# Optimization experiments

Hardware: AMD Instinct MI355X
Metric: run time of the kernel (lower is better)

Reference implementation:

```python
import jax, jax.numpy as jnp
import numpy as np

B, S, D = 4, 2048, 1024
HALF_PI = np.float32(np.pi / 2.0)


def setup_inputs() -> dict:
    key = jax.random.key(0)
    ks = jax.random.split(key, 12)
    std = np.float32(0.02)
    def w(k):
        return jax.random.normal(k, (D, D), dtype=jnp.float32) * std
    return {
        "x": jax.random.normal(ks[0], (B, S, D), dtype=jnp.float32),
        "W_q": w(ks[1]), "b_q": jnp.zeros((D,), jnp.float32),
        "W_k": w(ks[2]), "b_k": jnp.zeros((D,), jnp.float32),
        "W_v": w(ks[3]), "b_v": jnp.zeros((D,), jnp.float32),
        "W_t": w(ks[4]), "b_t": jnp.zeros((D,), jnp.float32),
        "W_o": w(ks[5]), "b_o": jnp.zeros((D,), jnp.float32),
        "entangle_strength": jnp.float32(0.5),
    }


def reference(x, W_q, b_q, W_k, b_k, W_v, b_v, W_t, b_t, W_o, b_o, entangle_strength):
    scale = jnp.float32(np.sqrt(D))
    Q = x @ W_q + b_q          # [B,S,D]
    K = x @ W_k + b_k
    V = x @ W_v + b_v
    # theta in [0, pi/2]; r = cos(2*theta)
    theta_q = jax.nn.sigmoid(Q @ W_t + b_t) * HALF_PI
    theta_k = jax.nn.sigmoid(K @ W_t + b_t) * HALF_PI
    r_q = jnp.cos(2.0 * theta_q)
    r_k = jnp.cos(2.0 * theta_k)
    classical = jnp.einsum("bqd,bkd->bqk", Q, K) / scale
    quantum = jnp.einsum("bqd,bkd->bqk", r_q, r_k) * entangle_strength
    attn_weights = jax.nn.softmax(classical + quantum, axis=-1)  # [B,S,S]
    # dropout: eval mode -> identity
    out = jnp.einsum("bqk,bkd->bqd", attn_weights, V)
    out = out @ W_o + b_o
    return out, attn_weights
```

## Files before the change

kernel.cpp:

```cpp
#include <hip/hip_runtime.h>
#include <cstdint>

typedef unsigned short u16;
typedef __attribute__((ext_vector_type(8))) short bf16x8;
typedef __attribute__((ext_vector_type(4))) float f32x4;

__device__ __forceinline__ u16 f2b(float x) {
  unsigned u = __float_as_uint(x);
  u += 0x7FFFu + ((u >> 16) & 1u);
  return (u16)(u >> 16);
}

__device__ __forceinline__ void gload16(const void* g, void* l) {
  __builtin_amdgcn_global_load_lds(
      (const __attribute__((address_space(1))) void*)g,
      (__attribute__((address_space(3))) void*)l, 16, 0, 0);
}

__device__ __forceinline__ int swz(int r) { return (r & 3) ^ ((r >> 2) & 3); }

template <int N>
__device__ __forceinline__ void vmwait() {
  if constexpr (N == 0) asm volatile("s_waitcnt vmcnt(0)" ::: "memory");
  else if constexpr (N == 3) asm volatile("s_waitcnt vmcnt(3)" ::: "memory");
  else if constexpr (N == 4) asm volatile("s_waitcnt vmcnt(4)" ::: "memory");
  else if constexpr (N == 6) asm volatile("s_waitcnt vmcnt(6)" ::: "memory");
  else if constexpr (N == 8) asm volatile("s_waitcnt vmcnt(8)" ::: "memory");
}

template <int L>
__device__ __forceinline__ void stage_region(const u16* __restrict__ G,
                                             long long ld, int gcol,
                                             u16* L_, int tid) {
#pragma unroll
  for (int j = 0; j < L; ++j) {
    const int P = j * 512 + tid;
    const int r = P >> 2;
    const int cl = (P & 3) ^ swz(r);
    gload16(G + (long long)r * ld + gcol + cl * 8, L_ + P * 8);
  }
}

__device__ __forceinline__ bf16x8 frag(const u16* reg_, int row, int cA) {
  return *(const bf16x8*)(reg_ + row * 32 + ((cA ^ swz(row)) << 3));
}

template <int EPI, int WM, int WN, int MR, int NR>
__global__ __launch_bounds__(512, 2) void g8p(
    const u16* __restrict__ A, long long lda, long long sAz,
    const u16* __restrict__ B, long long ldb, long long sBz,
    void* __restrict__ C0, void* __restrict__ C1, void* __restrict__ C2,
    long long ldc, long long sCz, int K,
    const float* __restrict__ b0, const float* __restrict__ b1,
    const float* __restrict__ b2, float preScale, const float* __restrict__ esp) {
  constexpr int BM = WM * MR * 16, BN = WN * NR * 16;
  constexpr int LA = BM / 128, LB = BN / 128;
  constexpr int AHALF = BM * 32;
  constexpr int BHALF = BN * 32;
  constexpr int BUFU = 2 * (AHALF + BHALF);
  constexpr int NH = NR / 2;
  __shared__ __align__(16) u16 lds[2 * BUFU];

  const int gx = gridDim.x, S = gx * gridDim.y;
  const int hw = blockIdx.y * gx + blockIdx.x;
  const int l = (hw & 7) * (S >> 3) + (hw >> 3);
  const int bx = l % gx, by = l / gx;
  const int z = blockIdx.z;
  const long long tM = (long long)by * BM;
  const long long tN = (long long)bx * BN;
  const u16* Ab = A + z * sAz + tM * lda;
  const u16* Bb = B + z * sBz + tN * ldb;
  const int tid = threadIdx.x;
  const int NT = K >> 6;

  stage_region<LA>(Ab, lda, 0,  lds, tid);
  stage_region<LB>(Bb, ldb, 0,  lds + 2 * AHALF, tid);
  stage_region<LA>(Ab, lda, 32, lds + AHALF, tid);
  stage_region<LB>(Bb, ldb, 32, lds + 2 * AHALF + BHALF, tid);
  stage_region<LA>(Ab, lda, 64, lds + BUFU, tid);
  stage_region<LB>(Bb, ldb, 64, lds + BUFU + 2 * AHALF, tid);
  vmwait<2 * (LA + LB)>();
  __builtin_amdgcn_s_barrier();

  const int wid = tid >> 6, lane = tid & 63;
  const int wm = wid / WN, wn = wid % WN;
  const int wr = wm * MR * 16, wc = wn * NR * 16;
  const int lr = lane & 15, cA = lane >> 4;
  f32x4 acc[MR][NR] = {};

  for (int t = 0; t < NT; ++t) {
    u16* bufc = lds + (t & 1) * BUFU;
    u16* bufn = lds + ((t + 1) & 1) * BUFU;
    const u16* Ak0p = bufc;
    const u16* Ak1p = bufc + AHALF;
    const u16* Bk0p = bufc + 2 * AHALF;
    const u16* Bk1p = bufc + 2 * AHALF + BHALF;
    bf16x8 a[MR], b[NH];

#pragma unroll
    for (int m = 0; m < MR; ++m) a[m] = frag(Ak0p, wr + m * 16 + lr, cA);
#pragma unroll
    for (int n = 0; n < NH; ++n) b[n] = frag(Bk0p, wc + n * 16 + lr, cA);
    if (t + 1 < NT)
      stage_region<LA>(Ab, lda, (t + 1) * 64 + 32, bufn + AHALF, tid);
    __builtin_amdgcn_s_barrier();
    asm volatile("s_waitcnt lgkmcnt(0)" ::: "memory");
    __builtin_amdgcn_s_setprio(1);
#pragma unroll
    for (int m = 0; m < MR; ++m)
#pragma unroll
      for (int n = 0; n < NH; ++n)
        acc[m][n] = __builtin_amdgcn_mfma_f32_16x16x32_bf16(a[m], b[n],
                                                            acc[m][n], 0, 0, 0);
    __builtin_amdgcn_s_setprio(0);
    __builtin_amdgcn_s_barrier();

#pragma unroll
    for (int n = 0; n < NH; ++n) b[n] = frag(Bk0p, wc + (NH + n) * 16 + lr, cA);
    if (t + 1 < NT)
      stage_region<LB>(Bb, ldb, (t + 1) * 64 + 32, bufn + 2 * AHALF + BHALF, tid);
    if (t < NT - 1) vmwait<2 * (LA + LB)>(); else vmwait<0>();
    __builtin_amdgcn_s_barrier();
    asm volatile("s_waitcnt lgkmcnt(0)" ::: "memory");
    __builtin_amdgcn_s_setprio(1);
#pragma unroll
    for (int m = 0; m < MR; ++m)
#pragma unroll
      for (int n = 0; n < NH; ++n)
        acc[m][NH + n] = __builtin_amdgcn_mfma_f32_16x16x32_bf16(
            a[m], b[n], acc[m][NH + n], 0, 0, 0);
    __builtin_amdgcn_s_setprio(0);
    __builtin_amdgcn_s_barrier();

#pragma unroll
    for (int m = 0; m < MR; ++m) a[m] = frag(Ak1p, wr + m * 16 + lr, cA);
#pragma unroll
    for (int n = 0; n < NH; ++n) b[n] = frag(Bk1p, wc + n * 16 + lr, cA);
    if (t + 2 < NT)
      stage_region<LA>(Ab, lda, (t + 2) * 64, bufc, tid);
    __builtin_amdgcn_s_barrier();
    asm volatile("s_waitcnt lgkmcnt(0)" ::: "memory");
    __builtin_amdgcn_s_setprio(1);
#pragma unroll
    for (int m = 0; m < MR; ++m)
#pragma unroll
      for (int n = 0; n < NH; ++n)
        acc[m][n] = __builtin_amdgcn_mfma_f32_16x16x32_bf16(a[m], b[n],
                                                            acc[m][n], 0, 0, 0);
    __builtin_amdgcn_s_setprio(0);
    __builtin_amdgcn_s_barrier();

#pragma unroll
    for (int n = 0; n < NH; ++n) b[n] = frag(Bk1p, wc + (NH + n) * 16 + lr, cA);
    if (t + 2 < NT)
      stage_region<LB>(Bb, ldb, (t + 2) * 64, bufc + 2 * AHALF, tid);
    if (t < NT - 2) vmwait<2 * (LA + LB)>();
    else if (t == NT - 2) vmwait<LA + LB>();
    __builtin_amdgcn_s_barrier();
    asm volatile("s_waitcnt lgkmcnt(0)" ::: "memory");
    __builtin_amdgcn_s_setprio(1);
#pragma unroll
    for (int m = 0; m < MR; ++m)
#pragma unroll
      for (int n = 0; n < NH; ++n)
        acc[m][NH + n] = __builtin_amdgcn_mfma_f32_16x16x32_bf16(
            a[m], b[n], acc[m][NH + n], 0, 0, 0);
    __builtin_amdgcn_s_setprio(0);
    __builtin_amdgcn_s_barrier();
  }

  const int rr = (lane >> 4) << 2;
  float ps = preScale, mul = 1.0f;
  if constexpr (EPI == 1) {
    ps = (z == 0) ? preScale : 1.0f;
    mul = (z == 0) ? esp[0] : 1.0f;
  }
#pragma unroll
  for (int m = 0; m < MR; ++m) {
#pragma unroll
    for (int n = 0; n < NR; ++n) {
      const int col = (int)tN + wc + n * 16 + lr;
#pragma unroll
      for (int r = 0; r < 4; ++r) {
        const long long row = tM + wr + m * 16 + rr + r;
        const float v = acc[m][n][r];
        if constexpr (EPI == 0) {
          const int g = col >> 10, cc = col & 1023;
          if (g == 0)      ((u16*)C0)[row * 2048 + cc] = f2b((v + b0[cc]) * 0.03125f);
          else if (g == 1) ((u16*)C1)[row * 2048 + cc] = f2b(v + b1[cc]);
          else             ((u16*)C2)[row * 1024 + cc] = f2b(v + b2[cc]);
        } else if constexpr (EPI == 1) {
          const float tt = v * ps + b0[col];
          const float sg = 1.f / (1.f + __expf(-tt));
          ((u16*)C0)[z * sCz + row * ldc + col] = f2b(mul * cospif(sg));
        } else if constexpr (EPI == 2) {
          ((u16*)C0)[z * sCz + row * ldc + col] = f2b(v);
        } else if constexpr (EPI == 3) {
          ((float*)C0)[z * sCz + row * ldc + col] = v + b0[col];
        } else {
          ((float*)C0)[z * sCz + row * ldc + col] = v;
        }
      }
    }
  }
}

__global__ __launch_bounds__(256) void softmax_rows(float* __restrict__ L,
                                                    u16* __restrict__ AB) {
  const long long row = blockIdx.x;
  float4* p4 = (float4*)(L + row * 2048);
  const int tid = threadIdx.x;
  float4 a = p4[tid], b = p4[tid + 256];
  float m = fmaxf(fmaxf(fmaxf(a.x, a.y), fmaxf(a.z, a.w)),
                  fmaxf(fmaxf(b.x, b.y), fmaxf(b.z, b.w)));
#pragma unroll
  for (int o = 32; o > 0; o >>= 1) m = fmaxf(m, __shfl_xor(m, o));
  __shared__ float rmax[4], rsum[4];
  const int wid = tid >> 6, lane = tid & 63;
  if (lane == 0) rmax[wid] = m;
  __syncthreads();
  m = fmaxf(fmaxf(rmax[0], rmax[1]), fmaxf(rmax[2], rmax[3]));
  a.x = __expf(a.x - m); a.y = __expf(a.y - m);
  a.z = __expf(a.z - m); a.w = __expf(a.w - m);
  b.x = __expf(b.x - m); b.y = __expf(b.y - m);
  b.z = __expf(b.z - m); b.w = __expf(b.w - m);
  float s = a.x + a.y + a.z + a.w + b.x + b.y + b.z + b.w;
#pragma unroll
  for (int o = 32; o > 0; o >>= 1) s += __shfl_xor(s, o);
  if (lane == 0) rsum[wid] = s;
  __syncthreads();
  s = rsum[0] + rsum[1] + rsum[2] + rsum[3];
  const float inv = 1.0f / s;
  a.x *= inv; a.y *= inv; a.z *= inv; a.w *= inv;
  b.x *= inv; b.y *= inv; b.z *= inv; b.w *= inv;
  p4[tid] = a;
  p4[tid + 256] = b;
  ushort4* o4 = (ushort4*)(AB + row * 2048);
  o4[tid]       = make_ushort4(f2b(a.x), f2b(a.y), f2b(a.z), f2b(a.w));
  o4[tid + 256] = make_ushort4(f2b(b.x), f2b(b.y), f2b(b.z), f2b(b.w));
}

__global__ __launch_bounds__(256) void cvt_x(const float* __restrict__ X,
                                             u16* __restrict__ XB) {
  const int i = blockIdx.x * 256 + threadIdx.x;
  float4 v = ((const float4*)X)[i];
  ((ushort4*)XB)[i] = make_ushort4(f2b(v.x), f2b(v.y), f2b(v.z), f2b(v.w));
}

__global__ void cvt_w(const float* __restrict__ W0, const float* __restrict__ W1,
                      const float* __restrict__ W2, const float* __restrict__ W3,
                      const float* __restrict__ W4, u16* __restrict__ WT) {
  __shared__ float t[32][33];
  const int z = blockIdx.z;
  const float* W = (z == 0) ? W0 : (z == 1) ? W1 : (z == 2) ? W2 : (z == 3) ? W3 : W4;
  u16* D = WT + (long long)z * 1024 * 1024;
  const int c0 = blockIdx.x * 32, r0 = blockIdx.y * 32;
  const int tx = threadIdx.x, ty = threadIdx.y;
#pragma unroll
  for (int i = 0; i < 4; ++i)
    t[ty + i * 8][tx] = W[(long long)(r0 + ty + i * 8) * 1024 + c0 + tx];
  __syncthreads();
#pragma unroll
  for (int i = 0; i < 4; ++i)
    D[(long long)(c0 + ty + i * 8) * 1024 + r0 + tx] = f2b(t[tx][ty + i * 8]);
}

__global__ void transpose_v(const u16* __restrict__ Vb, u16* __restrict__ VT) {
  __shared__ u16 t[32][33];
  const int b = blockIdx.z;
  const u16* V = Vb + (long long)b * 2048 * 1024;
  u16* O = VT + (long long)b * 1024 * 2048;
  const int d0 = blockIdx.x * 32, s0 = blockIdx.y * 32;
  const int tx = threadIdx.x, ty = threadIdx.y;
#pragma unroll
  for (int i = 0; i < 4; ++i)
    t[ty + i * 8][tx] = V[(long long)(s0 + ty + i * 8) * 1024 + d0 + tx];
  __syncthreads();
#pragma unroll
  for (int i = 0; i < 4; ++i)
    O[(long long)(d0 + ty + i * 8) * 2048 + s0 + tx] = t[tx][ty + i * 8];
}

extern "C" void kernel_launch(void* const* d_in, const int* in_sizes, int n_in,
                              void* d_out, int out_size, void* d_ws,
                              size_t ws_size, hipStream_t stream) {
  const float* x  = (const float*)d_in[0];
  const float* Wq = (const float*)d_in[1];
  const float* bq = (const float*)d_in[2];
  const float* Wk = (const float*)d_in[3];
  const float* bk = (const float*)d_in[4];
  const float* Wv = (const float*)d_in[5];
  const float* bv = (const float*)d_in[6];
  const float* Wt = (const float*)d_in[7];
  const float* bt = (const float*)d_in[8];
  const float* Wo = (const float*)d_in[9];
  const float* bo = (const float*)d_in[10];
  const float* es = (const float*)d_in[11];

  char* ws = (char*)d_ws;
  u16* WT   = (u16*)(ws);
  u16* XB   = (u16*)(ws + 10485760);
  u16* Qcat = (u16*)(ws + 27262976);
  u16* Kcat = Qcat + 16777216;
  u16* Vb   = (u16*)(ws + 94371840);
  u16* VT   = (u16*)(ws + 111149056);
  u16* WtT  = WT + 3 * 1048576;
  u16* WoT  = WT + 4 * 1048576;
  u16* ATT  = Qcat;
  u16* AV   = XB;

  float* outO = (float*)d_out;
  float* outA = outO + 8388608;

  cvt_x<<<8192, 256, 0, stream>>>(x, XB);
  cvt_w<<<dim3(32, 32, 5), dim3(32, 8), 0, stream>>>(Wq, Wk, Wv, Wt, Wo, WT);
  g8p<0, 4, 2, 2, 8><<<dim3(12, 64, 1), 512, 0, stream>>>(
      XB, 1024, 0, WT, 1024, 0, Qcat, Kcat, Vb, 0, 0, 1024, bq, bk, bv, 1.f, nullptr);
  g8p<1, 4, 2, 2, 8><<<dim3(4, 64, 2), 512, 0, stream>>>(
      Qcat, 2048, 16777216LL, WtT, 1024, 0, Qcat + 1024, nullptr, nullptr,
      2048, 16777216LL, 1024, bt, nullptr, nullptr, 32.f, es);
  transpose_v<<<dim3(32, 64, 4), dim3(32, 8), 0, stream>>>(Vb, VT);
  g8p<4, 2, 4, 8, 4><<<dim3(8, 8, 4), 512, 0, stream>>>(
      Qcat, 2048, 4194304LL, Kcat, 2048, 4194304LL, outA, nullptr, nullptr,
      2048, 4194304LL, 2048, nullptr, nullptr, nullptr, 1.f, nullptr);
  softmax_rows<<<8192, 256, 0, stream>>>(outA, ATT);
  g8p<2, 4, 2, 2, 8><<<dim3(4, 16, 4), 512, 0, stream>>>(
      ATT, 2048, 4194304LL, VT, 2048, 2097152LL, AV, nullptr, nullptr,
      1024, 2097152LL, 2048, nullptr, nullptr, nullptr, 1.f, nullptr);
  g8p<3, 4, 2, 2, 8><<<dim3(4, 64, 1), 512, 0, stream>>>(
      AV, 1024, 0, WoT, 1024, 0, outO, nullptr, nullptr,
      1024, 0, 1024, bo, nullptr, nullptr, 1.f, nullptr);
}
```

Baseline: 372.1 us.

## Restructure GEMM into quadrant-split tiles with 64-wide K chunks and 8-way swizzle

New measurement: 343.1 us. 7.8% less time.

```diff
diff --git a/kernel.cpp b/kernel.cpp
--- a/kernel.cpp
+++ b/kernel.cpp
@@ -16,8 +16,6 @@
       (const __attribute__((address_space(1))) void*)g,
       (__attribute__((address_space(3))) void*)l, 16, 0, 0);
 }
-
-__device__ __forceinline__ int swz(int r) { return (r & 3) ^ ((r >> 2) & 3); }
 
 template <int N>
 __device__ __forceinline__ void vmwait() {
@@ -29,37 +27,148 @@
 }
 
 template <int L>
-__device__ __forceinline__ void stage_region(const u16* __restrict__ G,
-                                             long long ld, int gcol,
-                                             u16* L_, int tid) {
+__device__ __forceinline__ void stage_half(const u16* __restrict__ G,
+                                           long long ld, int kb,
+                                           u16* Ldst, int tid) {
 #pragma unroll
   for (int j = 0; j < L; ++j) {
     const int P = j * 512 + tid;
-    const int r = P >> 2;
-    const int cl = (P & 3) ^ swz(r);
-    gload16(G + (long long)r * ld + gcol + cl * 8, L_ + P * 8);
-  }
-}
-
-__device__ __forceinline__ bf16x8 frag(const u16* reg_, int row, int cA) {
-  return *(const bf16x8*)(reg_ + row * 32 + ((cA ^ swz(row)) << 3));
-}
-
-template <int EPI, int WM, int WN, int MR, int NR>
-__global__ __launch_bounds__(512, 2) void g8p(
+    const int r = P >> 3, c = P & 7;
+    gload16(G + (long long)r * ld + kb + ((c ^ (r & 7)) << 3), Ldst + P * 8);
+  }
+}
+
+__device__ __forceinline__ bf16x8 fr8(const u16* R, int row, int chunk) {
+  return *(const bf16x8*)(R + row * 64 + ((chunk ^ (row & 7)) << 3));
+}
+
+template <int FM, int MODE>
+__device__ __forceinline__ void tile_body(
+    u16* cur, u16* oth, const u16* GA_lo, const u16* GA_hi,
+    const u16* GB_lo, const u16* GB_hi, long long lda, long long ldb,
+    int kb1, int kb2, int wm, int wn, int lr, int cA, int tid,
+    f32x4 (&acc)[2][2][FM][2]) {
+  constexpr int LA = FM / 2, LB = 2;
+  constexpr int AH = 2048 * FM, BH = 8192;
+  const u16* Alo = cur;
+  const u16* Ahi = cur + AH;
+  const u16* Blo = cur + 2 * AH;
+  const u16* Bhi = cur + 2 * AH + BH;
+  const int ar = wm * (FM * 16) + lr;
+  const int br = wn * 32 + lr;
+  bf16x8 a[FM][2], b[2][2];
+
+#pragma unroll
+  for (int f = 0; f < FM; ++f) {
+    a[f][0] = fr8(Alo, ar + f * 16, cA);
+    a[f][1] = fr8(Alo, ar + f * 16, 4 + cA);
+  }
+#pragma unroll
+  for (int g = 0; g < 2; ++g) {
+    b[g][0] = fr8(Blo, br + g * 16, cA);
+    b[g][1] = fr8(Blo, br + g * 16, 4 + cA);
+  }
+  if constexpr (MODE < 2) stage_half<LA>(GA_hi, lda, kb1, oth + AH, tid);
+  if constexpr (FM == 4) asm volatile("s_waitcnt lgkmcnt(8)" ::: "memory");
+  if constexpr (MODE < 2) vmwait<2 * LA + 2>(); else vmwait<0>();
+  __builtin_amdgcn_s_barrier();
+  asm volatile("s_waitcnt lgkmcnt(0)" ::: "memory");
+  __builtin_amdgcn_s_setprio(1);
+#pragma unroll
+  for (int kh = 0; kh < 2; ++kh)
+#pragma unroll
+    for (int f = 0; f < FM; ++f)
+#pragma unroll
+      for (int g = 0; g < 2; ++g)
+        acc[0][0][f][g] = __builtin_amdgcn_mfma_f32_16x16x32_bf16(
+            a[f][kh], b[g][kh], acc[0][0][f][g], 0, 0, 0);
+  __builtin_amdgcn_s_setprio(0);
+  __builtin_amdgcn_s_barrier();
+
+#pragma unroll
+  for (int g = 0; g < 2; ++g) {
+    b[g][0] = fr8(Bhi, br + g * 16, cA);
+    b[g][1] = fr8(Bhi, br + g * 16, 4 + cA);
+  }
+  if constexpr (MODE < 2) stage_half<LB>(GB_hi, ldb, kb1, oth + 2 * AH + BH, tid);
+  __builtin_amdgcn_s_barrier();
+  asm volatile("s_waitcnt lgkmcnt(0)" ::: "memory");
+  __builtin_amdgcn_s_setprio(1);
+#pragma unroll
+  for (int kh = 0; kh < 2; ++kh)
+#pragma unroll
+    for (int f = 0; f < FM; ++f)
+#pragma unroll
+      for (int g = 0; g < 2; ++g)
+        acc[0][1][f][g] = __builtin_amdgcn_mfma_f32_16x16x32_bf16(
+            a[f][kh], b[g][kh], acc[0][1][f][g], 0, 0, 0);
+  __builtin_amdgcn_s_setprio(0);
+  __builtin_amdgcn_s_barrier();
+
+#pragma unroll
+  for (int f = 0; f < FM; ++f) {
+    a[f][0] = fr8(Ahi, ar + f * 16, cA);
+    a[f][1] = fr8(Ahi, ar + f * 16, 4 + cA);
+  }
+#pragma unroll
+  for (int g = 0; g < 2; ++g) {
+    b[g][0] = fr8(Blo, br + g * 16, cA);
+    b[g][1] = fr8(Blo, br + g * 16, 4 + cA);
+  }
+  if constexpr (MODE == 0) stage_half<LA>(GA_lo, lda, kb2, cur, tid);
+  if constexpr (FM == 4) asm volatile("s_waitcnt lgkmcnt(8)" ::: "memory");
+  __builtin_amdgcn_s_barrier();
+  asm volatile("s_waitcnt lgkmcnt(0)" ::: "memory");
+  __builtin_amdgcn_s_setprio(1);
+#pragma unroll
+  for (int kh = 0; kh < 2; ++kh)
+#pragma unroll
+    for (int f = 0; f < FM; ++f)
+#pragma unroll
+      for (int g = 0; g < 2; ++g)
+        acc[1][0][f][g] = __builtin_amdgcn_mfma_f32_16x16x32_bf16(
+            a[f][kh], b[g][kh], acc[1][0][f][g], 0, 0, 0);
+  __builtin_amdgcn_s_setprio(0);
+  __builtin_amdgcn_s_barrier();
+
+#pragma unroll
+  for (int g = 0; g < 2; ++g) {
+    b[g][0] = fr8(Bhi, br + g * 16, cA);
+    b[g][1] = fr8(Bhi, br + g * 16, 4 + cA);
+  }
+  if constexpr (MODE == 0) stage_half<LB>(GB_lo, ldb, kb2, cur + 2 * AH, tid);
+  if constexpr (MODE == 0) vmwait<2 * LA + 4>();
+  else if constexpr (MODE == 1) vmwait<LA + 2>();
+  __builtin_amdgcn_s_barrier();
+  asm volatile("s_waitcnt lgkmcnt(0)" ::: "memory");
+  __builtin_amdgcn_s_setprio(1);
+#pragma unroll
+  for (int kh = 0; kh < 2; ++kh)
+#pragma unroll
+    for (int f = 0; f < FM; ++f)
+#pragma unroll
+      for (int g = 0; g < 2; ++g)
+        acc[1][1][f][g] = __builtin_amdgcn_mfma_f32_16x16x32_bf16(
+            a[f][kh], b[g][kh], acc[1][1][f][g], 0, 0, 0);
+  __builtin_amdgcn_s_setprio(0);
+  __builtin_amdgcn_s_barrier();
+}
+
+template <int EPI, int FM>
+__global__ __launch_bounds__(512, 2) void g8q(
     const u16* __restrict__ A, long long lda, long long sAz,
     const u16* __restrict__ B, long long ldb, long long sBz,
     void* __restrict__ C0, void* __restrict__ C1, void* __restrict__ C2,
     long long ldc, long long sCz, int K,
     const float* __restrict__ b0, const float* __restrict__ b1,
     const float* __restrict__ b2, float preScale, const float* __restrict__ esp) {
-  constexpr int BM = WM * MR * 16, BN = WN * NR * 16;
-  constexpr int LA = BM / 128, LB = BN / 128;
-  constexpr int AHALF = BM * 32;
-  constexpr int BHALF = BN * 32;
-  constexpr int BUFU = 2 * (AHALF + BHALF);
-  constexpr int NH = NR / 2;
+  constexpr int BM = 64 * FM;
+  constexpr int LA = FM / 2, LB = 2;
+  constexpr int AH = 2048 * FM, BH = 8192;
+  constexpr int BUFU = 2 * AH + 2 * BH;
   __shared__ __align__(16) u16 lds[2 * BUFU];
+  u16* buf0 = lds;
+  u16* buf1 = lds + BUFU;
 
   const int gx = gridDim.x, S = gx * gridDim.y;
   const int hw = blockIdx.y * gx + blockIdx.x;
@@ -67,107 +176,40 @@
   const int bx = l % gx, by = l / gx;
   const int z = blockIdx.z;
   const long long tM = (long long)by * BM;
-  const long long tN = (long long)bx * BN;
+  const long long tN = (long long)bx * 256;
   const u16* Ab = A + z * sAz + tM * lda;
   const u16* Bb = B + z * sBz + tN * ldb;
+  const u16* GA_lo = Ab;
+  const u16* GA_hi = Ab + (long long)(BM / 2) * lda;
+  const u16* GB_lo = Bb;
+  const u16* GB_hi = Bb + 128 * ldb;
   const int tid = threadIdx.x;
   const int NT = K >> 6;
 
-  stage_region<LA>(Ab, lda, 0,  lds, tid);
-  stage_region<LB>(Bb, ldb, 0,  lds + 2 * AHALF, tid);
-  stage_region<LA>(Ab, lda, 32, lds + AHALF, tid);
-  stage_region<LB>(Bb, ldb, 32, lds + 2 * AHALF + BHALF, tid);
-  stage_region<LA>(Ab, lda, 64, lds + BUFU, tid);
-  stage_region<LB>(Bb, ldb, 64, lds + BUFU + 2 * AHALF, tid);
-  vmwait<2 * (LA + LB)>();
+  stage_half<LA>(GA_lo, lda, 0, buf0, tid);
+  stage_half<LB>(GB_lo, ldb, 0, buf0 + 2 * AH, tid);
+  stage_half<LA>(GA_hi, lda, 0, buf0 + AH, tid);
+  stage_half<LB>(GB_hi, ldb, 0, buf0 + 2 * AH + BH, tid);
+  stage_half<LA>(GA_lo, lda, 64, buf1, tid);
+  stage_half<LB>(GB_lo, ldb, 64, buf1 + 2 * AH, tid);
+  vmwait<2 * LA + 4>();
   __builtin_amdgcn_s_barrier();
 
   const int wid = tid >> 6, lane = tid & 63;
-  const int wm = wid / WN, wn = wid % WN;
-  const int wr = wm * MR * 16, wc = wn * NR * 16;
+  const int wm = wid >> 2, wn = wid & 3;
   const int lr = lane & 15, cA = lane >> 4;
-  f32x4 acc[MR][NR] = {};
-
-  for (int t = 0; t < NT; ++t) {
-    u16* bufc = lds + (t & 1) * BUFU;
-    u16* bufn = lds + ((t + 1) & 1) * BUFU;
-    const u16* Ak0p = bufc;
-    const u16* Ak1p = bufc + AHALF;
-    const u16* Bk0p = bufc + 2 * AHALF;
-    const u16* Bk1p = bufc + 2 * AHALF + BHALF;
-    bf16x8 a[MR], b[NH];
-
-#pragma unroll
-    for (int m = 0; m < MR; ++m) a[m] = frag(Ak0p, wr + m * 16 + lr, cA);
-#pragma unroll
-    for (int n = 0; n < NH; ++n) b[n] = frag(Bk0p, wc + n * 16 + lr, cA);
-    if (t + 1 < NT)
-      stage_region<LA>(Ab, lda, (t + 1) * 64 + 32, bufn + AHALF, tid);
-    __builtin_amdgcn_s_barrier();
-    asm volatile("s_waitcnt lgkmcnt(0)" ::: "memory");
-    __builtin_amdgcn_s_setprio(1);
-#pragma unroll
-    for (int m = 0; m < MR; ++m)
-#pragma unroll
-      for (int n = 0; n < NH; ++n)
-        acc[m][n] = __builtin_amdgcn_mfma_f32_16x16x32_bf16(a[m], b[n],
-                                                            acc[m][n], 0, 0, 0);
-    __builtin_amdgcn_s_setprio(0);
-    __builtin_amdgcn_s_barrier();
-
-#pragma unroll
-    for (int n = 0; n < NH; ++n) b[n] = frag(Bk0p, wc + (NH + n) * 16 + lr, cA);
-    if (t + 1 < NT)
-      stage_region<LB>(Bb, ldb, (t + 1) * 64 + 32, bufn + 2 * AHALF + BHALF, tid);
-    if (t < NT - 1) vmwait<2 * (LA + LB)>(); else vmwait<0>();
-    __builtin_amdgcn_s_barrier();
-    asm volatile("s_waitcnt lgkmcnt(0)" ::: "memory");
-    __builtin_amdgcn_s_setprio(1);
-#pragma unroll
-    for (int m = 0; m < MR; ++m)
-#pragma unroll
-      for (int n = 0; n < NH; ++n)
-        acc[m][NH + n] = __builtin_amdgcn_mfma_f32_16x16x32_bf16(
-            a[m], b[n], acc[m][NH + n], 0, 0, 0);
-    __builtin_amdgcn_s_setprio(0);
-    __builtin_amdgcn_s_barrier();
-
-#pragma unroll
-    for (int m = 0; m < MR; ++m) a[m] = frag(Ak1p, wr + m * 16 + lr, cA);
-#pragma unroll
-    for (int n = 0; n < NH; ++n) b[n] = frag(Bk1p, wc + n * 16 + lr, cA);
-    if (t + 2 < NT)
-      stage_region<LA>(Ab, lda, (t + 2) * 64, bufc, tid);
-    __builtin_amdgcn_s_barrier();
-    asm volatile("s_waitcnt lgkmcnt(0)" ::: "memory");
-    __builtin_amdgcn_s_setprio(1);
-#pragma unroll
-    for (int m = 0; m < MR; ++m)
-#pragma unroll
-      for (int n = 0; n < NH; ++n)
-        acc[m][n] = __builtin_amdgcn_mfma_f32_16x16x32_bf16(a[m], b[n],
-                                                            acc[m][n], 0, 0, 0);
-    __builtin_amdgcn_s_setprio(0);
-    __builtin_amdgcn_s_barrier();
-
-#pragma unroll
-    for (int n = 0; n < NH; ++n) b[n] = frag(Bk1p, wc + (NH + n) * 16 + lr, cA);
-    if (t + 2 < NT)
-      stage_region<LB>(Bb, ldb, (t + 2) * 64, bufc + 2 * AHALF, tid);
-    if (t < NT - 2) vmwait<2 * (LA + LB)>();
-    else if (t == NT - 2) vmwait<LA + LB>();
-    __builtin_amdgcn_s_barrier();
-    asm volatile("s_waitcnt lgkmcnt(0)" ::: "memory");
-    __builtin_amdgcn_s_setprio(1);
-#pragma unroll
-    for (int m = 0; m < MR; ++m)
-#pragma unroll
-      for (int n = 0; n < NH; ++n)
-        acc[m][NH + n] = __builtin_amdgcn_mfma_f32_16x16x32_bf16(
-            a[m], b[n], acc[m][NH + n], 0, 0, 0);
-    __builtin_amdgcn_s_setprio(0);
-    __builtin_amdgcn_s_barrier();
-  }
+  f32x4 acc[2][2][FM][2] = {};
+
+  for (int t = 0; t + 2 < NT; t += 2) {
+    tile_body<FM, 0>(buf0, buf1, GA_lo, GA_hi, GB_lo, GB_hi, lda, ldb,
+                     (t + 1) * 64, (t + 2) * 64, wm, wn, lr, cA, tid, acc);
+    tile_body<FM, 0>(buf1, buf0, GA_lo, GA_hi, GB_lo, GB_hi, lda, ldb,
+                     (t + 2) * 64, (t + 3) * 64, wm, wn, lr, cA, tid, acc);
+  }
+  tile_body<FM, 1>(buf0, buf1, GA_lo, GA_hi, GB_lo, GB_hi, lda, ldb,
+                   (NT - 1) * 64, 0, wm, wn, lr, cA, tid, acc);
+  tile_body<FM, 2>(buf1, buf0, GA_lo, GA_hi, GB_lo, GB_hi, lda, ldb,
+                   0, 0, wm, wn, lr, cA, tid, acc);
 
   const int rr = (lane >> 4) << 2;
   float ps = preScale, mul = 1.0f;
@@ -176,29 +218,37 @@
     mul = (z == 0) ? esp[0] : 1.0f;
   }
 #pragma unroll
-  for (int m = 0; m < MR; ++m) {
-#pragma unroll
-    for (int n = 0; n < NR; ++n) {
-      const int col = (int)tN + wc + n * 16 + lr;
-#pragma unroll
-      for (int r = 0; r < 4; ++r) {
-        const long long row = tM + wr + m * 16 + rr + r;
-        const float v = acc[m][n][r];
-        if constexpr (EPI == 0) {
-          const int g = col >> 10, cc = col & 1023;
-          if (g == 0)      ((u16*)C0)[row * 2048 + cc] = f2b((v + b0[cc]) * 0.03125f);
-          else if (g == 1) ((u16*)C1)[row * 2048 + cc] = f2b(v + b1[cc]);
-          else             ((u16*)C2)[row * 1024 + cc] = f2b(v + b2[cc]);
-        } else if constexpr (EPI == 1) {
-          const float tt = v * ps + b0[col];
-          const float sg = 1.f / (1.f + __expf(-tt));
-          ((u16*)C0)[z * sCz + row * ldc + col] = f2b(mul * cospif(sg));
-        } else if constexpr (EPI == 2) {
-          ((u16*)C0)[z * sCz + row * ldc + col] = f2b(v);
-        } else if constexpr (EPI == 3) {
-          ((float*)C0)[z * sCz + row * ldc + col] = v + b0[col];
-        } else {
-          ((float*)C0)[z * sCz + row * ldc + col] = v;
+  for (int mh = 0; mh < 2; ++mh) {
+#pragma unroll
+    for (int nh = 0; nh < 2; ++nh) {
+#pragma unroll
+      for (int f = 0; f < FM; ++f) {
+#pragma unroll
+        for (int g = 0; g < 2; ++g) {
+          const int col = (int)tN + nh * 128 + wn * 32 + g * 16 + lr;
+          const f32x4 vv = acc[mh][nh][f][g];
+#pragma unroll
+          for (int r = 0; r < 4; ++r) {
+            const long long row =
+                tM + mh * (BM / 2) + wm * (FM * 16) + f * 16 + rr + r;
+            const float v = vv[r];
+            if constexpr (EPI == 0) {
+              const int gg = col >> 10, cc = col & 1023;
+              if (gg == 0)      ((u16*)C0)[row * 2048 + cc] = f2b((v + b0[cc]) * 0.03125f);
+              else if (gg == 1) ((u16*)C1)[row * 2048 + cc] = f2b(v + b1[cc]);
+              else              ((u16*)C2)[row * 1024 + cc] = f2b(v + b2[cc]);
+            } else if constexpr (EPI == 1) {
+              const float tt = v * ps + b0[col];
+              const float sg = 1.f / (1.f + __expf(-tt));
+              ((u16*)C0)[z * sCz + row * ldc + col] = f2b(mul * cospif(sg));
+            } else if constexpr (EPI == 2) {
+              ((u16*)C0)[z * sCz + row * ldc + col] = f2b(v);
+            } else if constexpr (EPI == 3) {
+              ((float*)C0)[z * sCz + row * ldc + col] = v + b0[col];
+            } else {
+              ((float*)C0)[z * sCz + row * ldc + col] = v;
+            }
+          }
         }
       }
     }
@@ -314,20 +364,20 @@
 
   cvt_x<<<8192, 256, 0, stream>>>(x, XB);
   cvt_w<<<dim3(32, 32, 5), dim3(32, 8), 0, stream>>>(Wq, Wk, Wv, Wt, Wo, WT);
-  g8p<0, 4, 2, 2, 8><<<dim3(12, 64, 1), 512, 0, stream>>>(
+  g8q<0, 2><<<dim3(12, 64, 1), 512, 0, stream>>>(
       XB, 1024, 0, WT, 1024, 0, Qcat, Kcat, Vb, 0, 0, 1024, bq, bk, bv, 1.f, nullptr);
-  g8p<1, 4, 2, 2, 8><<<dim3(4, 64, 2), 512, 0, stream>>>(
+  g8q<1, 2><<<dim3(4, 64, 2), 512, 0, stream>>>(
       Qcat, 2048, 16777216LL, WtT, 1024, 0, Qcat + 1024, nullptr, nullptr,
       2048, 16777216LL, 1024, bt, nullptr, nullptr, 32.f, es);
   transpose_v<<<dim3(32, 64, 4), dim3(32, 8), 0, stream>>>(Vb, VT);
-  g8p<4, 2, 4, 8, 4><<<dim3(8, 8, 4), 512, 0, stream>>>(
+  g8q<4, 4><<<dim3(8, 8, 4), 512, 0, stream>>>(
       Qcat, 2048, 4194304LL, Kcat, 2048, 4194304LL, outA, nullptr, nullptr,
       2048, 4194304LL, 2048, nullptr, nullptr, nullptr, 1.f, nullptr);
   softmax_rows<<<8192, 256, 0, stream>>>(outA, ATT);
-  g8p<2, 4, 2, 2, 8><<<dim3(4, 16, 4), 512, 0, stream>>>(
+  g8q<2, 2><<<dim3(4, 16, 4), 512, 0, stream>>>(
       ATT, 2048, 4194304LL, VT, 2048, 2097152LL, AV, nullptr, nullptr,
       1024, 2097152LL, 2048, nullptr, nullptr, nullptr, 1.f, nullptr);
-  g8p<3, 4, 2, 2, 8><<<dim3(4, 64, 1), 512, 0, stream>>>(
+  g8q<3, 2><<<dim3(4, 64, 1), 512, 0, stream>>>(
       AV, 1024, 0, WoT, 1024, 0, outO, nullptr, nullptr,
       1024, 0, 1024, bo, nullptr, nullptr, 1.f, nullptr);
 }
```
